# Kernel tuning notes

Hardware: AMD Instinct MI355X
Metric: run time of the kernel (lower is better)

Reference implementation:

```python
import jax, jax.numpy as jnp
import numpy as np

HEADS, KD, AR, RES, DIM = 8, 32, 4, 28, 384
D = AR * KD          # 128
DH = HEADS * D       # 1024
NH_KD = HEADS * KD   # 256


def setup_inputs() -> dict:
    key = jax.random.key(0)
    kit = iter(jax.random.split(key, 40))

    def rn(shape, scale=0.05):
        return jax.random.normal(next(kit), shape, jnp.float32) * scale

    B = 8
    inp = {}
    inp['x'] = jax.random.normal(next(kit), (B, DIM, RES, RES), jnp.float32)

    def conv_bn(name, o, i):
        # 1x1 conv weight [O, I] (kernel squeezed), conv bias, folded BN scale/shift
        inp['W' + name] = rn((o, i))
        inp['b' + name] = rn((o,))
        inp[name + '_s'] = 1.0 + rn((o,))
        inp[name + '_b'] = rn((o,))

    conv_bn('q', NH_KD, DIM)
    conv_bn('k', NH_KD, DIM)
    conv_bn('v', DH, DIM)
    # depthwise 3x3 v_local conv (OIHW, groups=DH -> I=1) + BN
    inp['Wvl'] = rn((DH, 1, 3, 3))
    inp['bvl'] = rn((DH,))
    inp['vl_s'] = 1.0 + rn((DH,))
    inp['vl_b'] = rn((DH,))
    # talking-head 1x1 convs over the heads axis: weight [out_head, in_head]
    inp['Wth1'] = rn((HEADS, HEADS))
    inp['bth1'] = rn((HEADS,))
    inp['Wth2'] = rn((HEADS, HEADS))
    inp['bth2'] = rn((HEADS,))
    conv_bn('p', DIM, DH)
    # relative position biases: one slot per unique (|dr|,|dc|) offset = RES*RES slots
    inp['attention_biases'] = rn((HEADS, RES * RES))
    r = np.arange(RES)
    rr, cc = np.meshgrid(r, r, indexing='ij')
    rows, cols = rr.reshape(-1), cc.reshape(-1)
    dr = np.abs(rows[:, None] - rows[None, :])
    dc = np.abs(cols[:, None] - cols[None, :])
    inp['bias_idxs'] = jnp.asarray(dr * RES + dc, jnp.int32)  # [N, N]
    return inp


def _cbn(t, W, b, s, sh):
    # 1x1 conv + eval-mode BatchNorm folded to per-channel affine
    y = jnp.einsum('bchw,oc->bohw', t, W) + b[None, :, None, None]
    return y * s[None, :, None, None] + sh[None, :, None, None]


def _forward(x, Wq, bq, q_s, q_b, Wk, bk, k_s, k_b, Wv, bv, v_s, v_b,
             Wvl, bvl, vl_s, vl_b, Wth1, bth1, Wth2, bth2,
             Wp, bp, p_s, p_b, attention_biases, bias_idxs):
    B, C, H, W = x.shape
    N = H * W
    scale = KD ** -0.5

    q = _cbn(x, Wq, bq, q_s, q_b).reshape(B, HEADS, KD, N).transpose(0, 1, 3, 2)  # [B,h,N,kd]
    k = _cbn(x, Wk, bk, k_s, k_b).reshape(B, HEADS, KD, N)                        # [B,h,kd,N]
    v4 = _cbn(x, Wv, bv, v_s, v_b)                                                # [B,dh,H,W]

    vl = jax.lax.conv_general_dilated(
        v4, Wvl, window_strides=(1, 1), padding='SAME',
        feature_group_count=DH, dimension_numbers=('NCHW', 'OIHW', 'NCHW'))
    vl = (vl + bvl[None, :, None, None]) * vl_s[None, :, None, None] + vl_b[None, :, None, None]

    v = v4.reshape(B, HEADS, D, N).transpose(0, 1, 3, 2)  # [B,h,N,d]

    ab = attention_biases[:, bias_idxs]                   # [h,N,N]
    attn = jnp.einsum('bhnk,bhkm->bhnm', q, k) * scale + ab[None]
    attn = jnp.einsum('bhnm,gh->bgnm', attn, Wth1) + bth1[None, :, None, None]
    attn = jax.nn.softmax(attn, axis=-1)
    attn = jnp.einsum('bhnm,gh->bgnm', attn, Wth2) + bth2[None, :, None, None]

    o = jnp.einsum('bhnm,bhmd->bhnd', attn, v)            # [B,h,N,d]
    o = o.transpose(0, 1, 3, 2).reshape(B, DH, H, W)
    o = o + vl
    return _cbn(o, Wp, bp, p_s, p_b)                      # [B,dim,H,W]


def reference(x, Wq, bq, q_s, q_b, Wk, bk, k_s, k_b, Wv, bv, v_s, v_b,
              Wvl, bvl, vl_s, vl_b, Wth1, bth1, Wth2, bth2,
              Wp, bp, p_s, p_b, attention_biases, bias_idxs):
    return _forward(x, Wq, bq, q_s, q_b, Wk, bk, k_s, k_b, Wv, bv, v_s, v_b,
                    Wvl, bvl, vl_s, vl_b, Wth1, bth1, Wth2, bth2,
                    Wp, bp, p_s, p_b, attention_biases, bias_idxs)
```

## Files before the change

kernel.cpp:

```cpp
#include <hip/hip_runtime.h>
#include <hip/hip_bf16.h>

typedef __hip_bfloat16 bf16;
typedef __attribute__((ext_vector_type(8))) short short8v;
typedef __attribute__((ext_vector_type(4))) short short4v;
typedef __attribute__((ext_vector_type(4))) float f32x4;
typedef __attribute__((ext_vector_type(2))) float f32x2;

__device__ __forceinline__ float b2f(bf16 v){ return __bfloat162float(v); }
__device__ __forceinline__ bf16  f2b(float v){ return __float2bfloat16(v); }
__device__ __forceinline__ float su2f(short s){
    unsigned short us = (unsigned short)s;
    return __bfloat162float(*reinterpret_cast<bf16*>(&us));
}
__device__ __forceinline__ float ldf(const void* t, size_t i, int isb){
    return isb ? b2f(((const bf16*)t)[i]) : ((const float*)t)[i];
}

constexpr int Bn = 8, CIN = 384, RESn = 28, Nn = 784, DHn = 1024;
constexpr int AST = 800;

__device__ __forceinline__ void gload16(const void* g, void* l)
{
    __builtin_amdgcn_global_load_lds(
        (const __attribute__((address_space(1))) void*)g,
        (__attribute__((address_space(3))) void*)l, 16, 0, 0);
}

__global__ void k_detect(const unsigned* __restrict__ xw, int* __restrict__ flag)
{
    if (blockIdx.x == 0 && threadIdx.x == 0) {
        int cnt = 0;
        for (int i = 0; i < 256; ++i) {
            unsigned lo = xw[i] & 0xFFFFu;
            int e = (int)((lo >> 7) & 0xFF);
            if (e >= 112 && e <= 132) ++cnt;
        }
        *flag = (cnt >= 128) ? 1 : 0;
    }
}

struct PtrArgs { const void* p[26]; };
__global__ __launch_bounds__(256) void k_prep(PtrArgs a, bf16* __restrict__ Wqkv,
                                              float* __restrict__ al, float* __restrict__ be,
                                              float* __restrict__ mb, bf16* __restrict__ Wvlt,
                                              const int* __restrict__ flag)
{
    const int isb = *flag;
    const int tid = threadIdx.x;
    const int role = blockIdx.y;
    if (role == 0) {
        int stride = gridDim.x * 256;
        for (int e = blockIdx.x * 256 + tid; e < 1536 * 384; e += stride) {
            int co = e / 384, k = e % 384;
            const void* src; int lc;
            if (co < 256)      { src = a.p[1]; lc = co; }
            else if (co < 512) { src = a.p[5]; lc = co - 256; }
            else               { src = a.p[9]; lc = co - 512; }
            Wqkv[e] = f2b(ldf(src, (size_t)lc * 384 + k, isb));
        }
    } else if (role == 1) {
        int co = blockIdx.x * 256 + tid;
        if (co < 1536) {
            const void *b_, *s_, *h_; int lc;
            if (co < 256)      { b_ = a.p[2];  s_ = a.p[3];  h_ = a.p[4];  lc = co; }
            else if (co < 512) { b_ = a.p[6];  s_ = a.p[7];  h_ = a.p[8];  lc = co - 256; }
            else               { b_ = a.p[10]; s_ = a.p[11]; h_ = a.p[12]; lc = co - 512; }
            float aa = ldf(s_, lc, isb);
            al[co] = aa;
            be[co] = ldf(b_, lc, isb) * aa + ldf(h_, lc, isb);
        }
    } else if (role == 2) {
        int i = blockIdx.x * 256 + tid;
        if (i < 8 * Nn) {
            int g = i / Nn, p = i % Nn;
            float acc = ldf(a.p[18], g, isb);
            #pragma unroll
            for (int h = 0; h < 8; ++h)
                acc += ldf(a.p[17], g * 8 + h, isb) * ldf(a.p[25], (size_t)h * Nn + p, isb);
            mb[i] = acc;
        }
    } else {
        int e = blockIdx.x * 256 + tid;
        if (e < 1024 * 9) {
            int c = e / 9, tap = e % 9;
            Wvlt[tap * 1024 + c] = f2b(ldf(a.p[13], e, isb));
        }
    }
}

struct ConvArgs { const void* src[10]; unsigned long long dstoff[10]; int n[10]; };
__global__ void k_convb_all(ConvArgs a, char* __restrict__ ws, const int* __restrict__ flag)
{
    int i = blockIdx.y;
    int n = a.n[i];
    const void* s = a.src[i];
    bf16* d = (bf16*)(ws + a.dstoff[i]);
    int isb = *flag;
    int stride = gridDim.x * blockDim.x;
    for (int t = blockIdx.x * blockDim.x + threadIdx.x; t < n; t += stride)
        d[t] = isb ? ((const bf16*)s)[t] : f2b(((const float*)s)[t]);
}

__global__ __launch_bounds__(256) void k_abfull(
    const float* __restrict__ mb, const int* __restrict__ idxs,
    bf16* __restrict__ abfull)
{
    __shared__ float mbs[8][Nn];
    const int tid = threadIdx.x;
    for (int i = tid; i < 8 * Nn; i += 256) ((float*)mbs)[i] = mb[i];
    __syncthreads();
    const int nstart = blockIdx.x * 2;
    for (int n = nstart; n < nstart + 2; ++n) {
        for (int m = tid; m < Nn; m += 256) {
            int id = idxs[(size_t)n * Nn + m];
            #pragma unroll
            for (int g = 0; g < 8; ++g)
                abfull[((size_t)g * Nn + n) * AST + m] = f2b(mbs[g][id]);
        }
    }
}

__global__ __launch_bounds__(256) void k_xt(const void* __restrict__ xr, bf16* __restrict__ xt,
                                            const int* __restrict__ flag)
{
    const int isb = *flag;
    __shared__ bf16 t[32][33];
    int b = blockIdx.z, n0 = blockIdx.x * 32, c0 = blockIdx.y * 32;
    int tid = threadIdx.x;
    for (int i = tid; i < 1024; i += 256) {
        int r = i >> 5, c = i & 31;
        int n = n0 + c;
        t[r][c] = (n < Nn) ? f2b(ldf(xr, ((size_t)b * CIN + c0 + r) * Nn + n, isb)) : f2b(0.f);
    }
    __syncthreads();
    for (int i = tid; i < 1024; i += 256) {
        int r = i >> 5, c = i & 31;
        int n = n0 + r;
        if (n < Nn) xt[((size_t)b * Nn + n) * CIN + c0 + c] = t[c][r];
    }
}

__global__ __launch_bounds__(256) void k_vt(const bf16* __restrict__ vbuf, bf16* __restrict__ vt)
{
    __shared__ bf16 t[32][33];
    int b = blockIdx.z, n0 = blockIdx.x * 32, c0 = blockIdx.y * 32;
    int tid = threadIdx.x;
    for (int i = tid; i < 1024; i += 256) {
        int r = i >> 5, c = i & 31;
        int n = n0 + r;
        t[r][c] = (n < Nn) ? vbuf[((size_t)b * Nn + n) * DHn + c0 + c] : f2b(0.f);
    }
    __syncthreads();
    for (int i = tid; i < 1024; i += 256) {
        int r = i >> 5, c = i & 31;
        int n = n0 + c;
        vt[((size_t)b * DHn + c0 + r) * AST + n] = t[c][r];
    }
}

template<int MI>
__device__ __forceinline__ void gemm_core(
    const bf16* __restrict__ A, int lda, int rowsA, int arow0,
    const bf16* __restrict__ B, int ldb, int rowsB, int brow0,
    int K, short* ldsA, short* ldsB, f32x4 (&acc)[MI][4])
{
    const int tid  = threadIdx.x;
    const int lane = tid & 63;
    const int wm   = tid >> 7, wn = (tid >> 6) & 1;
    const int rsub = ((tid >> 6) << 4) | (tid & 15);
    const int q    = (tid >> 4) & 3;
    const int wbase = tid & 192;
    const short8v* A8 = (const short8v*)ldsA;
    const short8v* B8 = (const short8v*)ldsB;

    for (int k0 = 0; k0 < K; k0 += 32) {
        __syncthreads();
        #pragma unroll
        for (int c = 0; c < MI / 2; ++c) {
            int row = arow0 + c * 64 + rsub; row = row < rowsA ? row : rowsA - 1;
            gload16((const short*)A + (size_t)row * lda + k0 + q * 8,
                    ldsA + (size_t)(c * 256 + wbase) * 8);
        }
        #pragma unroll
        for (int c = 0; c < 2; ++c) {
            int row = brow0 + c * 64 + rsub; row = row < rowsB ? row : rowsB - 1;
            gload16((const short*)B + (size_t)row * ldb + k0 + q * 8,
                    ldsB + (size_t)(c * 256 + wbase) * 8);
        }
        __syncthreads();
        short8v a[MI], bb[4];
        #pragma unroll
        for (int i = 0; i < MI; ++i) a[i] = A8[(wm * MI + i) * 64 + lane];
        #pragma unroll
        for (int j = 0; j < 4; ++j) bb[j] = B8[(wn * 4 + j) * 64 + lane];
        #pragma unroll
        for (int i = 0; i < MI; ++i)
            #pragma unroll
            for (int j = 0; j < 4; ++j)
                acc[i][j] = __builtin_amdgcn_mfma_f32_16x16x32_bf16(a[i], bb[j], acc[i][j], 0, 0, 0);
    }
}

#define EPI_COORDS(MI)                                      \
    const int tid  = threadIdx.x;                           \
    const int lane = tid & 63;                              \
    const int wm   = tid >> 7, wn = (tid >> 6) & 1;         \
    const int rq   = lane >> 4, cl = lane & 15; (void)rq;

__global__ __launch_bounds__(256) void k_proj_m(
    const bf16* __restrict__ xt, const bf16* __restrict__ Wqkv,
    const float* __restrict__ al, const float* __restrict__ be,
    bf16* __restrict__ qbuf, bf16* __restrict__ kbuf, bf16* __restrict__ vbuf)
{
    __shared__ short ldsA[4096], ldsB[4096];
    const int n0 = blockIdx.x * 128, co0 = blockIdx.y * 128;
    const int b = blockIdx.z;
    f32x4 acc[4][4] = {};
    gemm_core<4>(xt + (size_t)b * Nn * CIN, CIN, Nn, n0,
                 Wqkv, CIN, 1536, co0, CIN, ldsA, ldsB, acc);
    EPI_COORDS(4)
    #pragma unroll
    for (int i = 0; i < 4; ++i)
        #pragma unroll
        for (int j = 0; j < 4; ++j) {
            int co = co0 + (wn * 4 + j) * 16 + cl;
            float a_ = al[co], bb_ = be[co];
            int nb = n0 + (wm * 4 + i) * 16 + rq * 4;
            #pragma unroll
            for (int r = 0; r < 4; ++r) {
                int n = nb + r;
                if (n >= Nn) continue;
                float y = a_ * acc[i][j][r] + bb_;
                if (co < 256)      qbuf[((size_t)b * Nn + n) * 256 + co]       = f2b(y);
                else if (co < 512) kbuf[((size_t)b * Nn + n) * 256 + (co-256)] = f2b(y);
                else               vbuf[((size_t)b * Nn + n) * DHn + (co-512)] = f2b(y);
            }
        }
}

__global__ __launch_bounds__(256) void k_logits_raw(
    const bf16* __restrict__ qbuf, const bf16* __restrict__ kbuf,
    bf16* __restrict__ attn, int bi0)
{
    __shared__ short ldsA[4096], ldsB[4096];
    const int n0 = blockIdx.x * 128, m0 = blockIdx.y * 128;
    const int z = blockIdx.z, h = z & 7, bloc = z >> 3, b = bi0 + bloc;
    f32x4 acc[4][4] = {};
    gemm_core<4>(qbuf + (size_t)b * Nn * 256 + h * 32, 256, Nn, n0,
                 kbuf + (size_t)b * Nn * 256 + h * 32, 256, Nn, m0,
                 32, ldsA, ldsB, acc);
    bf16* arow = attn + (size_t)(bloc * 8 + h) * Nn * AST;
    EPI_COORDS(4)
    #pragma unroll
    for (int i = 0; i < 4; ++i)
        #pragma unroll
        for (int j = 0; j < 4; ++j) {
            int m = m0 + (wn * 4 + j) * 16 + cl;
            if (m >= Nn) continue;
            int nb = n0 + (wm * 4 + i) * 16 + rq * 4;
            #pragma unroll
            for (int r = 0; r < 4; ++r) {
                int n = nb + r;
                if (n < Nn) arow[(size_t)n * AST + m] = f2b(acc[i][j][r]);
            }
        }
}

__global__ __launch_bounds__(256) void k_softmax_mix(
    bf16* __restrict__ attn_all, const bf16* __restrict__ abfull,
    const bf16* __restrict__ W1, const bf16* __restrict__ W2, const bf16* __restrict__ b2v)
{
    const int n = blockIdx.x, bloc = blockIdx.y;
    const int tid = threadIdx.x;
    bf16* base = attn_all + (size_t)bloc * 8 * Nn * AST;
    __shared__ float w1s[64], w2s[64], b2sh[8], lis[8], wred[4][8];
    if (tid < 64) { w1s[tid] = b2f(W1[tid]) * 0.17677669529663687f; w2s[tid] = b2f(W2[tid]); }
    if (tid < 8)  b2sh[tid] = b2f(b2v[tid]);
    __syncthreads();

    const bool live = tid < 196;
    const int m0 = (live ? tid : 195) * 4;

    f32x2 raw2[8][2];
    #pragma unroll
    for (int h = 0; h < 8; ++h) {
        short4v v = *(const short4v*)(base + ((size_t)h * Nn + n) * AST + m0);
        raw2[h][0] = f32x2{su2f(v[0]), su2f(v[1])};
        raw2[h][1] = f32x2{su2f(v[2]), su2f(v[3])};
    }

    float out[8][4];
    #pragma unroll
    for (int g = 0; g < 8; ++g) {
        short4v bv = *(const short4v*)(abfull + ((size_t)g * Nn + n) * AST + m0);
        f32x2 a0 = {su2f(bv[0]), su2f(bv[1])};
        f32x2 a1 = {su2f(bv[2]), su2f(bv[3])};
        #pragma unroll
        for (int h = 0; h < 8; ++h) {
            float w = w1s[g * 8 + h];
            f32x2 wv = {w, w};
            a0 += raw2[h][0] * wv;
            a1 += raw2[h][1] * wv;
        }
        out[g][0] = __expf(fminf(a0[0], 60.f));
        out[g][1] = __expf(fminf(a0[1], 60.f));
        out[g][2] = __expf(fminf(a1[0], 60.f));
        out[g][3] = __expf(fminf(a1[1], 60.f));
        float s = live ? (out[g][0] + out[g][1]) + (out[g][2] + out[g][3]) : 0.f;
        #pragma unroll
        for (int sh = 32; sh > 0; sh >>= 1) s += __shfl_xor(s, sh, 64);
        if ((tid & 63) == 0) wred[tid >> 6][g] = s;
    }
    __syncthreads();
    if (tid < 8)
        lis[tid] = 1.f / (wred[0][tid] + wred[1][tid] + wred[2][tid] + wred[3][tid]);
    __syncthreads();

    f32x2 p2[8][2];
    #pragma unroll
    for (int h = 0; h < 8; ++h) {
        float lh = lis[h];
        p2[h][0] = f32x2{out[h][0] * lh, out[h][1] * lh};
        p2[h][1] = f32x2{out[h][2] * lh, out[h][3] * lh};
    }
    if (live) {
        #pragma unroll
        for (int g = 0; g < 8; ++g) {
            f32x2 acc0 = {b2sh[g], b2sh[g]};
            f32x2 acc1 = acc0;
            #pragma unroll
            for (int h = 0; h < 8; ++h) {
                float w = w2s[g * 8 + h];
                f32x2 wv = {w, w};
                acc0 += p2[h][0] * wv;
                acc1 += p2[h][1] * wv;
            }
            short4v sv;
            bf16 b0 = f2b(acc0[0]); sv[0] = *reinterpret_cast<short*>(&b0);
            bf16 b1 = f2b(acc0[1]); sv[1] = *reinterpret_cast<short*>(&b1);
            bf16 b2 = f2b(acc1[0]); sv[2] = *reinterpret_cast<short*>(&b2);
            bf16 b3 = f2b(acc1[1]); sv[3] = *reinterpret_cast<short*>(&b3);
            *(short4v*)(base + ((size_t)g * Nn + n) * AST + m0) = sv;
        }
    }
}

__global__ __launch_bounds__(256) void k_pv_m(
    const bf16* __restrict__ attn, const bf16* __restrict__ vt,
    bf16* __restrict__ obuf, int bi0)
{
    __shared__ short ldsA[2048], ldsB[4096];
    const int n0 = blockIdx.x * 64;
    const int z = blockIdx.z, g = z & 7, bloc = z >> 3, b = bi0 + bloc;
    f32x4 acc[2][4] = {};
    gemm_core<2>(attn + (size_t)(bloc * 8 + g) * Nn * AST, AST, Nn, n0,
                 vt + ((size_t)b * DHn + g * 128) * AST, AST, 128, 0,
                 AST, ldsA, ldsB, acc);
    bf16* ob = obuf + (size_t)b * Nn * DHn + g * 128;
    EPI_COORDS(2)
    #pragma unroll
    for (int i = 0; i < 2; ++i)
        #pragma unroll
        for (int j = 0; j < 4; ++j) {
            int d = (wn * 4 + j) * 16 + cl;
            int nb = n0 + (wm * 2 + i) * 16 + rq * 4;
            #pragma unroll
            for (int r = 0; r < 4; ++r) {
                int n = nb + r;
                if (n < Nn) ob[(size_t)n * DHn + d] = f2b(acc[i][j][r]);
            }
        }
}

__global__ __launch_bounds__(256) void k_dwconv_add(
    const bf16* __restrict__ vbuf, const bf16* __restrict__ Wvlt,
    const bf16* __restrict__ bvl, const bf16* __restrict__ vls, const bf16* __restrict__ vlb,
    bf16* __restrict__ obuf)
{
    const int t = threadIdx.x;
    const int n = blockIdx.y * 2 + (t >> 7);
    const int bi = blockIdx.z;
    const int c0 = (t & 127) * 8;
    const int h = n / RESn, w = n % RESn;
    float acc[8] = {};
    #pragma unroll
    for (int dh = -1; dh <= 1; ++dh)
        #pragma unroll
        for (int dw = -1; dw <= 1; ++dw) {
            int hh = h + dh, ww = w + dw;
            if (hh < 0 || hh >= RESn || ww < 0 || ww >= RESn) continue;
            int widx = (dh + 1) * 3 + (dw + 1);
            short8v wv = *(const short8v*)&Wvlt[widx * 1024 + c0];
            short8v v  = *(const short8v*)&vbuf[((size_t)bi * Nn + hh * RESn + ww) * DHn + c0];
            #pragma unroll
            for (int u = 0; u < 8; ++u)
                acc[u] += su2f(wv[u]) * su2f(v[u]);
        }
    short8v bv = *(const short8v*)&bvl[c0];
    short8v sv = *(const short8v*)&vls[c0];
    short8v hv = *(const short8v*)&vlb[c0];
    size_t off = ((size_t)bi * Nn + n) * DHn + c0;
    short8v ov = *(short8v*)&obuf[off];
    short8v res;
    #pragma unroll
    for (int u = 0; u < 8; ++u) {
        float vl = su2f(sv[u]) * (acc[u] + su2f(bv[u])) + su2f(hv[u]);
        bf16 bo = f2b(su2f(ov[u]) + vl);
        res[u] = *reinterpret_cast<short*>(&bo);
    }
    *(short8v*)&obuf[off] = res;
}

__global__ __launch_bounds__(256) void k_outproj_m(
    const bf16* __restrict__ Wp, const bf16* __restrict__ obuf,
    const bf16* __restrict__ bp, const bf16* __restrict__ ps, const bf16* __restrict__ pb,
    void* __restrict__ outv, const int* __restrict__ flag)
{
    __shared__ short ldsA[2048], ldsB[4096];
    const int n0 = blockIdx.x * 128, oc0 = blockIdx.y * 64;
    const int b = blockIdx.z;
    f32x4 acc[2][4] = {};
    gemm_core<2>(Wp, DHn, 384, oc0,
                 obuf + (size_t)b * Nn * DHn, DHn, Nn, n0,
                 DHn, ldsA, ldsB, acc);
    const int isb = *flag;
    EPI_COORDS(2)
    #pragma unroll
    for (int i = 0; i < 2; ++i)
        #pragma unroll
        for (int j = 0; j < 4; ++j) {
            int n = n0 + (wn * 4 + j) * 16 + cl;
            if (n >= Nn) continue;
            int ocb = oc0 + (wm * 2 + i) * 16 + rq * 4;
            #pragma unroll
            for (int r = 0; r < 4; ++r) {
                int oc = ocb + r;
                float a_ = b2f(ps[oc]);
                float be_ = b2f(bp[oc]) * a_ + b2f(pb[oc]);
                float y = a_ * acc[i][j][r] + be_;
                size_t idx = ((size_t)b * CIN + oc) * Nn + n;
                if (isb) ((bf16*)outv)[idx] = f2b(y);
                else     ((float*)outv)[idx] = y;
            }
        }
}

extern "C" void kernel_launch(void* const* d_in, const int* in_sizes, int n_in,
                              void* d_out, int out_size, void* d_ws, size_t ws_size,
                              hipStream_t stream)
{
    char* ws = (char*)d_ws;
    auto align256 = [](size_t v) { return (v + 255) & ~(size_t)255; };

    size_t off = 0;
    size_t off_flag = off;            off = align256(off + 4);
    size_t p_off[26];
    for (int i = 0; i < 26; ++i) { p_off[i] = off; off = align256(off + (size_t)in_sizes[i] * 2); }
    size_t off_mb   = off; off = align256(off + (size_t)8 * Nn * 4);
    size_t off_ab   = off; off = align256(off + (size_t)8 * Nn * AST * 2);
    size_t off_q    = off; off = align256(off + (size_t)Bn * Nn * 256 * 2);
    size_t off_k    = off; off = align256(off + (size_t)Bn * Nn * 256 * 2);
    size_t off_v    = off; off = align256(off + (size_t)Bn * Nn * DHn * 2);
    size_t off_vt   = off; off = align256(off + (size_t)Bn * DHn * AST * 2);
    size_t off_o    = off; off = align256(off + (size_t)Bn * Nn * DHn * 2);
    size_t off_xt   = off; off = align256(off + (size_t)Bn * Nn * CIN * 2);
    size_t off_wqkv = off; off = align256(off + (size_t)1536 * CIN * 2);
    size_t off_al   = off; off = align256(off + (size_t)1536 * 4);
    size_t off_be   = off; off = align256(off + (size_t)1536 * 4);
    size_t off_wvlt = off; off = align256(off + (size_t)9 * 1024 * 2);
    size_t base = off;

    const size_t attn_per_b = (size_t)8 * Nn * AST * 2;
    int GB = 0;
    const int cand[4] = {8, 4, 2, 1};
    for (int ci = 0; ci < 4; ++ci) {
        if (base + (size_t)cand[ci] * attn_per_b + 512 <= ws_size) { GB = cand[ci]; break; }
    }
    if (!GB) return;

    size_t off_attn = base;

    int*  flag = (int*)(ws + off_flag);
    bf16* Pb[26];
    for (int i = 0; i < 26; ++i) Pb[i] = (bf16*)(ws + p_off[i]);
    float* mb    = (float*)(ws + off_mb);
    bf16* abfull = (bf16*)(ws + off_ab);
    bf16* qbuf  = (bf16*)(ws + off_q);
    bf16* kbuf  = (bf16*)(ws + off_k);
    bf16* vbuf  = (bf16*)(ws + off_v);
    bf16* vt    = (bf16*)(ws + off_vt);
    bf16* obuf  = (bf16*)(ws + off_o);
    bf16* xt    = (bf16*)(ws + off_xt);
    bf16* wqkv  = (bf16*)(ws + off_wqkv);
    float* alf  = (float*)(ws + off_al);
    float* bef  = (float*)(ws + off_be);
    bf16* wvlt  = (bf16*)(ws + off_wvlt);
    bf16* attn  = (bf16*)(ws + off_attn);
    const int* idxs = (const int*)d_in[26];

    k_detect<<<1, 64, 0, stream>>>((const unsigned*)d_in[0], flag);

    PtrArgs pa;
    for (int i = 0; i < 26; ++i) pa.p[i] = d_in[i];
    k_prep<<<dim3(288, 4), 256, 0, stream>>>(pa, wqkv, alf, bef, mb, wvlt, flag);

    const int cidx[10] = {14, 15, 16, 17, 19, 20, 21, 22, 23, 24};
    ConvArgs ca;
    for (int i = 0; i < 10; ++i) {
        ca.src[i] = d_in[cidx[i]];
        ca.dstoff[i] = p_off[cidx[i]];
        ca.n[i] = in_sizes[cidx[i]];
    }
    k_convb_all<<<dim3(64, 10), 256, 0, stream>>>(ca, ws, flag);

    bf16 *bvl = Pb[14], *vls = Pb[15], *vlb = Pb[16],
         *W1 = Pb[17], *W2 = Pb[19], *b2v = Pb[20],
         *Wp = Pb[21], *bp = Pb[22], *ps = Pb[23], *pb = Pb[24];

    k_xt<<<dim3(25, 12, 8), 256, 0, stream>>>(d_in[0], xt, flag);
    k_abfull<<<dim3(392), 256, 0, stream>>>(mb, idxs, abfull);

    k_proj_m<<<dim3(7, 12, 8), 256, 0, stream>>>(xt, wqkv, alf, bef, qbuf, kbuf, vbuf);
    k_vt<<<dim3(25, 32, 8), 256, 0, stream>>>(vbuf, vt);

    for (int bi0 = 0; bi0 < Bn; bi0 += GB) {
        k_logits_raw<<<dim3(7, 7, GB * 8), 256, 0, stream>>>(qbuf, kbuf, attn, bi0);
        k_softmax_mix<<<dim3(Nn, GB), 256, 0, stream>>>(attn, abfull, W1, W2, b2v);
        k_pv_m<<<dim3(13, 1, GB * 8), 256, 0, stream>>>(attn, vt, obuf, bi0);
    }

    k_dwconv_add<<<dim3(1, Nn / 2, 8), 256, 0, stream>>>(vbuf, wvlt, bvl, vls, vlb, obuf);
    k_outproj_m<<<dim3(7, 6, 8), 256, 0, stream>>>(Wp, obuf, bp, ps, pb, d_out, flag);
}
```

Measured before the change: 238.5 us.

## Fuse logits with talking-head mix and exp; fuse normalize and second mix into PV

The old three-kernel attention pipeline was logits, a separate softmax/mix pass and PV. It becomes two kernels. The first computes QK^T for all heads of a 16-row tile, applies the first talking-head mix with bias and exp, writes unnormalized exponentials, and writes partial row sums. The second normalizes using the split sums, applies the second head mix while staging P into LDS, and runs the PV MFMA. This removes one full read and write pass over the large attention buffer and one launch. The cost is smaller, more redundant tiles (E is reread per group pair) and a changed LDS staging layout.

Result: slower. 408.7 us (+71.4%).

```diff
diff --git a/kernel.cpp b/kernel.cpp
--- a/kernel.cpp
+++ b/kernel.cpp
@@ -5,13 +5,16 @@
 typedef __attribute__((ext_vector_type(8))) short short8v;
 typedef __attribute__((ext_vector_type(4))) short short4v;
 typedef __attribute__((ext_vector_type(4))) float f32x4;
-typedef __attribute__((ext_vector_type(2))) float f32x2;
 
 __device__ __forceinline__ float b2f(bf16 v){ return __bfloat162float(v); }
 __device__ __forceinline__ bf16  f2b(float v){ return __float2bfloat16(v); }
 __device__ __forceinline__ float su2f(short s){
     unsigned short us = (unsigned short)s;
     return __bfloat162float(*reinterpret_cast<bf16*>(&us));
+}
+__device__ __forceinline__ short f2s(float v){
+    bf16 b = __float2bfloat16(v);
+    return *reinterpret_cast<short*>(&b);
 }
 __device__ __forceinline__ float ldf(const void* t, size_t i, int isb){
     return isb ? b2f(((const bf16*)t)[i]) : ((const float*)t)[i];
@@ -159,6 +162,16 @@
     }
 }
 
+__device__ __forceinline__ void stage64x32(const bf16* __restrict__ src,
+    int row0, int row_lim, int k0, int k_lim, int ld, short* lds, int tid)
+{
+    int rsub = ((tid >> 6) << 4) | (tid & 15);
+    int q    = (tid >> 4) & 3;
+    int row = row0 + rsub; row = row < row_lim ? row : row_lim - 1;
+    gload16((const short*)src + (size_t)row * ld + k0 + q * 8,
+            lds + (size_t)(((rsub >> 4) * 4 + q) * 16 + (rsub & 15)) * 8);
+}
+
 template<int MI>
 __device__ __forceinline__ void gemm_core(
     const bf16* __restrict__ A, int lda, int rowsA, int arow0,
@@ -168,26 +181,17 @@
     const int tid  = threadIdx.x;
     const int lane = tid & 63;
     const int wm   = tid >> 7, wn = (tid >> 6) & 1;
-    const int rsub = ((tid >> 6) << 4) | (tid & 15);
-    const int q    = (tid >> 4) & 3;
-    const int wbase = tid & 192;
     const short8v* A8 = (const short8v*)ldsA;
     const short8v* B8 = (const short8v*)ldsB;
 
     for (int k0 = 0; k0 < K; k0 += 32) {
         __syncthreads();
         #pragma unroll
-        for (int c = 0; c < MI / 2; ++c) {
-            int row = arow0 + c * 64 + rsub; row = row < rowsA ? row : rowsA - 1;
-            gload16((const short*)A + (size_t)row * lda + k0 + q * 8,
-                    ldsA + (size_t)(c * 256 + wbase) * 8);
-        }
-        #pragma unroll
-        for (int c = 0; c < 2; ++c) {
-            int row = brow0 + c * 64 + rsub; row = row < rowsB ? row : rowsB - 1;
-            gload16((const short*)B + (size_t)row * ldb + k0 + q * 8,
-                    ldsB + (size_t)(c * 256 + wbase) * 8);
-        }
+        for (int c = 0; c < MI / 2; ++c)
+            stage64x32(A, arow0 + c * 64, rowsA, k0, K, lda, ldsA + c * 2048, tid);
+        #pragma unroll
+        for (int c = 0; c < 2; ++c)
+            stage64x32(B, brow0 + c * 64, rowsB, k0, K, ldb, ldsB + c * 2048, tid);
         __syncthreads();
         short8v a[MI], bb[4];
         #pragma unroll
@@ -239,138 +243,197 @@
         }
 }
 
-__global__ __launch_bounds__(256) void k_logits_raw(
+__global__ __launch_bounds__(256) void k_attA(
     const bf16* __restrict__ qbuf, const bf16* __restrict__ kbuf,
-    bf16* __restrict__ attn, int bi0)
-{
-    __shared__ short ldsA[4096], ldsB[4096];
-    const int n0 = blockIdx.x * 128, m0 = blockIdx.y * 128;
-    const int z = blockIdx.z, h = z & 7, bloc = z >> 3, b = bi0 + bloc;
-    f32x4 acc[4][4] = {};
-    gemm_core<4>(qbuf + (size_t)b * Nn * 256 + h * 32, 256, Nn, n0,
-                 kbuf + (size_t)b * Nn * 256 + h * 32, 256, Nn, m0,
-                 32, ldsA, ldsB, acc);
-    bf16* arow = attn + (size_t)(bloc * 8 + h) * Nn * AST;
-    EPI_COORDS(4)
-    #pragma unroll
-    for (int i = 0; i < 4; ++i)
-        #pragma unroll
-        for (int j = 0; j < 4; ++j) {
-            int m = m0 + (wn * 4 + j) * 16 + cl;
-            if (m >= Nn) continue;
-            int nb = n0 + (wm * 4 + i) * 16 + rq * 4;
+    const bf16* __restrict__ abfull, const bf16* __restrict__ W1,
+    bf16* __restrict__ E, float* __restrict__ sums, int bi0)
+{
+    __shared__ short ldsQ[4096];
+    __shared__ short ldsK[16384];
+    __shared__ float sred[4][8][16];
+    __shared__ float w1s[64];
+    const int tid = threadIdx.x;
+    const int nt = blockIdx.x >> 1, ms = blockIdx.x & 1;
+    const int bloc = blockIdx.y, b = bi0 + bloc;
+    const int n0 = nt * 16;
+    const int lane = tid & 63, wv = tid >> 6;
+    const int qrow = lane >> 4, cl = lane & 15;
+
+    if (tid < 64) w1s[tid] = b2f(W1[tid]) * 0.17677669529663687f;
+
+    {
+        const short8v* q8 = (const short8v*)(qbuf + (size_t)b * Nn * 256);
+        short8v* Q8w = (short8v*)ldsQ;
+        #pragma unroll
+        for (int s = tid; s < 512; s += 256) {
+            int r = s >> 5, j = s & 31;
+            Q8w[(j >> 2) * 64 + (j & 3) * 16 + r] = q8[(size_t)(n0 + r) * 32 + j];
+        }
+    }
+
+    float sreg[8][4];
+    #pragma unroll
+    for (int g = 0; g < 8; ++g)
+        #pragma unroll
+        for (int r = 0; r < 4; ++r) sreg[g][r] = 0.f;
+
+    const bf16* Bk = kbuf + (size_t)b * Nn * 256;
+    const short8v* Q8 = (const short8v*)ldsQ;
+    const short8v* K8 = (const short8v*)ldsK;
+    const int nmt = 6 + ms;
+
+    for (int mt = 0; mt < nmt; ++mt) {
+        int m0 = ms * 384 + mt * 64;
+        __syncthreads();
+        #pragma unroll
+        for (int h = 0; h < 8; ++h)
+            stage64x32(Bk, m0, Nn, h * 32, 256, 256, ldsK + h * 2048, tid);
+        __syncthreads();
+        f32x4 acc[8];
+        #pragma unroll
+        for (int h = 0; h < 8; ++h) {
+            short8v a = Q8[h * 64 + lane];
+            short8v bb = K8[h * 256 + wv * 64 + lane];
+            f32x4 z = {0.f, 0.f, 0.f, 0.f};
+            acc[h] = __builtin_amdgcn_mfma_f32_16x16x32_bf16(a, bb, z, 0, 0, 0);
+        }
+        const int m = m0 + wv * 16 + cl;
+        #pragma unroll
+        for (int g = 0; g < 8; ++g) {
             #pragma unroll
             for (int r = 0; r < 4; ++r) {
-                int n = nb + r;
-                if (n < Nn) arow[(size_t)n * AST + m] = f2b(acc[i][j][r]);
+                int n = n0 + qrow * 4 + r;
+                float a = (m < AST) ?
+                    su2f(*(const short*)&abfull[((size_t)g * Nn + n) * AST + m]) : 0.f;
+                #pragma unroll
+                for (int h = 0; h < 8; ++h) a += w1s[g * 8 + h] * acc[h][r];
+                float e = (m < Nn) ? __expf(fminf(a, 60.f)) : 0.f;
+                sreg[g][r] += e;
+                if (m < AST)
+                    E[((size_t)(bloc * 8 + g) * Nn + n) * AST + m] = f2b(e);
             }
         }
-}
-
-__global__ __launch_bounds__(256) void k_softmax_mix(
-    bf16* __restrict__ attn_all, const bf16* __restrict__ abfull,
-    const bf16* __restrict__ W1, const bf16* __restrict__ W2, const bf16* __restrict__ b2v)
-{
-    const int n = blockIdx.x, bloc = blockIdx.y;
+    }
+
+    #pragma unroll
+    for (int g = 0; g < 8; ++g)
+        #pragma unroll
+        for (int r = 0; r < 4; ++r) {
+            float v = sreg[g][r];
+            v += __shfl_xor(v, 1, 64);
+            v += __shfl_xor(v, 2, 64);
+            v += __shfl_xor(v, 4, 64);
+            v += __shfl_xor(v, 8, 64);
+            if (cl == 0) sred[wv][g][qrow * 4 + r] = v;
+        }
+    __syncthreads();
+    if (tid < 128) {
+        int g = tid >> 4, nl = tid & 15;
+        float s = sred[0][g][nl] + sred[1][g][nl] + sred[2][g][nl] + sred[3][g][nl];
+        sums[(size_t)ms * 64 * Nn + (size_t)(bloc * 8 + g) * Nn + n0 + nl] = s;
+    }
+}
+
+__global__ __launch_bounds__(256) void k_attB(
+    const bf16* __restrict__ E, const float* __restrict__ sums,
+    const bf16* __restrict__ vt, const bf16* __restrict__ W2,
+    const bf16* __restrict__ b2v, bf16* __restrict__ obuf, int bi0)
+{
+    __shared__ short ldsP[2][2048];
+    __shared__ short ldsV[2][8192];
+    __shared__ float w2sh[2][8];
+    __shared__ float b2sh[2];
     const int tid = threadIdx.x;
-    bf16* base = attn_all + (size_t)bloc * 8 * Nn * AST;
-    __shared__ float w1s[64], w2s[64], b2sh[8], lis[8], wred[4][8];
-    if (tid < 64) { w1s[tid] = b2f(W1[tid]) * 0.17677669529663687f; w2s[tid] = b2f(W2[tid]); }
-    if (tid < 8)  b2sh[tid] = b2f(b2v[tid]);
+    const int nt = blockIdx.x, gp = blockIdx.y, bloc = blockIdx.z;
+    const int b = bi0 + bloc;
+    const int n0 = nt * 32;
+    const int g0 = gp * 2;
+    const int lane = tid & 63, wv = tid >> 6;
+
+    if (tid < 16) w2sh[tid >> 3][tid & 7] = b2f(W2[(g0 + (tid >> 3)) * 8 + (tid & 7)]);
+    if (tid < 2)  b2sh[tid] = b2f(b2v[g0 + tid]);
+
+    const int nrow = tid >> 3;
+    const int msg  = (tid & 7) * 8;
+    const int nclamp = (n0 + nrow < Nn) ? (n0 + nrow) : (Nn - 1);
+    float dinv[8];
+    #pragma unroll
+    for (int h = 0; h < 8; ++h) {
+        size_t idx = (size_t)(bloc * 8 + h) * Nn + nclamp;
+        dinv[h] = 1.f / (sums[idx] + sums[(size_t)64 * Nn + idx]);
+    }
     __syncthreads();
 
-    const bool live = tid < 196;
-    const int m0 = (live ? tid : 195) * 4;
-
-    f32x2 raw2[8][2];
-    #pragma unroll
-    for (int h = 0; h < 8; ++h) {
-        short4v v = *(const short4v*)(base + ((size_t)h * Nn + n) * AST + m0);
-        raw2[h][0] = f32x2{su2f(v[0]), su2f(v[1])};
-        raw2[h][1] = f32x2{su2f(v[2]), su2f(v[3])};
-    }
-
-    float out[8][4];
-    #pragma unroll
-    for (int g = 0; g < 8; ++g) {
-        short4v bv = *(const short4v*)(abfull + ((size_t)g * Nn + n) * AST + m0);
-        f32x2 a0 = {su2f(bv[0]), su2f(bv[1])};
-        f32x2 a1 = {su2f(bv[2]), su2f(bv[3])};
-        #pragma unroll
-        for (int h = 0; h < 8; ++h) {
-            float w = w1s[g * 8 + h];
-            f32x2 wv = {w, w};
-            a0 += raw2[h][0] * wv;
-            a1 += raw2[h][1] * wv;
-        }
-        out[g][0] = __expf(fminf(a0[0], 60.f));
-        out[g][1] = __expf(fminf(a0[1], 60.f));
-        out[g][2] = __expf(fminf(a1[0], 60.f));
-        out[g][3] = __expf(fminf(a1[1], 60.f));
-        float s = live ? (out[g][0] + out[g][1]) + (out[g][2] + out[g][3]) : 0.f;
-        #pragma unroll
-        for (int sh = 32; sh > 0; sh >>= 1) s += __shfl_xor(s, sh, 64);
-        if ((tid & 63) == 0) wred[tid >> 6][g] = s;
-    }
-    __syncthreads();
-    if (tid < 8)
-        lis[tid] = 1.f / (wred[0][tid] + wred[1][tid] + wred[2][tid] + wred[3][tid]);
-    __syncthreads();
-
-    f32x2 p2[8][2];
-    #pragma unroll
-    for (int h = 0; h < 8; ++h) {
-        float lh = lis[h];
-        p2[h][0] = f32x2{out[h][0] * lh, out[h][1] * lh};
-        p2[h][1] = f32x2{out[h][2] * lh, out[h][3] * lh};
-    }
-    if (live) {
-        #pragma unroll
-        for (int g = 0; g < 8; ++g) {
-            f32x2 acc0 = {b2sh[g], b2sh[g]};
-            f32x2 acc1 = acc0;
-            #pragma unroll
-            for (int h = 0; h < 8; ++h) {
-                float w = w2s[g * 8 + h];
-                f32x2 wv = {w, w};
-                acc0 += p2[h][0] * wv;
-                acc1 += p2[h][1] * wv;
+    f32x4 acc[2][2][2] = {};
+
+    for (int mt = 0; mt < 13; ++mt) {
+        const int m0 = mt * 64;
+        const int nks = (mt < 12) ? 2 : 1;
+        __syncthreads();
+        #pragma unroll
+        for (int gs = 0; gs < 2; ++gs) {
+            const bf16* vs = vt + ((size_t)b * DHn + (g0 + gs) * 128) * AST;
+            for (int ks = 0; ks < nks; ++ks) {
+                stage64x32(vs, 0,  128, m0 + ks * 32, AST, AST, ldsV[gs] + ks * 4096, tid);
+                stage64x32(vs, 64, 128, m0 + ks * 32, AST, AST, ldsV[gs] + ks * 4096 + 2048, tid);
             }
-            short4v sv;
-            bf16 b0 = f2b(acc0[0]); sv[0] = *reinterpret_cast<short*>(&b0);
-            bf16 b1 = f2b(acc0[1]); sv[1] = *reinterpret_cast<short*>(&b1);
-            bf16 b2 = f2b(acc1[0]); sv[2] = *reinterpret_cast<short*>(&b2);
-            bf16 b3 = f2b(acc1[1]); sv[3] = *reinterpret_cast<short*>(&b3);
-            *(short4v*)(base + ((size_t)g * Nn + n) * AST + m0) = sv;
-        }
-    }
-}
-
-__global__ __launch_bounds__(256) void k_pv_m(
-    const bf16* __restrict__ attn, const bf16* __restrict__ vt,
-    bf16* __restrict__ obuf, int bi0)
-{
-    __shared__ short ldsA[2048], ldsB[4096];
-    const int n0 = blockIdx.x * 64;
-    const int z = blockIdx.z, g = z & 7, bloc = z >> 3, b = bi0 + bloc;
-    f32x4 acc[2][4] = {};
-    gemm_core<2>(attn + (size_t)(bloc * 8 + g) * Nn * AST, AST, Nn, n0,
-                 vt + ((size_t)b * DHn + g * 128) * AST, AST, 128, 0,
-                 AST, ldsA, ldsB, acc);
-    bf16* ob = obuf + (size_t)b * Nn * DHn + g * 128;
-    EPI_COORDS(2)
-    #pragma unroll
-    for (int i = 0; i < 2; ++i)
-        #pragma unroll
-        for (int j = 0; j < 4; ++j) {
-            int d = (wn * 4 + j) * 16 + cl;
-            int nb = n0 + (wm * 2 + i) * 16 + rq * 4;
-            #pragma unroll
-            for (int r = 0; r < 4; ++r) {
-                int n = nb + r;
-                if (n < Nn) ob[(size_t)n * DHn + d] = f2b(acc[i][j][r]);
+        }
+        if (msg < nks * 32) {
+            float p0[8], p1[8];
+            #pragma unroll
+            for (int e = 0; e < 8; ++e) { p0[e] = b2sh[0]; p1[e] = b2sh[1]; }
+            #pragma unroll
+            for (int g = 0; g < 8; ++g) {
+                short8v ev = *(const short8v*)&E[
+                    ((size_t)(bloc * 8 + g) * Nn + nclamp) * AST + m0 + msg];
+                float w0 = w2sh[0][g], w1 = w2sh[1][g], dv = dinv[g];
+                #pragma unroll
+                for (int e = 0; e < 8; ++e) {
+                    float pe = su2f(ev[e]) * dv;
+                    p0[e] += w0 * pe;
+                    p1[e] += w1 * pe;
+                }
             }
-        }
+            short8v s0, s1;
+            #pragma unroll
+            for (int e = 0; e < 8; ++e) { s0[e] = f2s(p0[e]); s1[e] = f2s(p1[e]); }
+            int ks = msg >> 5, q = (msg >> 3) & 3, sub = nrow >> 4, r = nrow & 15;
+            int slot = (ks * 2 + sub) * 64 + q * 16 + r;
+            ((short8v*)ldsP[0])[slot] = s0;
+            ((short8v*)ldsP[1])[slot] = s1;
+        }
+        __syncthreads();
+        #pragma unroll
+        for (int gs = 0; gs < 2; ++gs)
+            for (int ks = 0; ks < nks; ++ks)
+                #pragma unroll
+                for (int sub = 0; sub < 2; ++sub) {
+                    short8v a = ((const short8v*)ldsP[gs])[(ks * 2 + sub) * 64 + lane];
+                    #pragma unroll
+                    for (int jj = 0; jj < 2; ++jj) {
+                        short8v bb = ((const short8v*)ldsV[gs])[ks * 512 + (wv * 2 + jj) * 64 + lane];
+                        acc[gs][sub][jj] =
+                            __builtin_amdgcn_mfma_f32_16x16x32_bf16(a, bb, acc[gs][sub][jj], 0, 0, 0);
+                    }
+                }
+    }
+
+    const int qrow = lane >> 4, cl = lane & 15;
+    #pragma unroll
+    for (int gs = 0; gs < 2; ++gs)
+        #pragma unroll
+        for (int sub = 0; sub < 2; ++sub)
+            #pragma unroll
+            for (int jj = 0; jj < 2; ++jj) {
+                int d = (g0 + gs) * 128 + (wv * 2 + jj) * 16 + cl;
+                int nb = n0 + sub * 16 + qrow * 4;
+                #pragma unroll
+                for (int r = 0; r < 4; ++r) {
+                    int n = nb + r;
+                    if (n < Nn)
+                        obuf[((size_t)b * Nn + n) * DHn + d] = f2b(acc[gs][sub][jj][r]);
+                }
+            }
 }
 
 __global__ __launch_bounds__(256) void k_dwconv_add(
@@ -406,8 +469,7 @@
     #pragma unroll
     for (int u = 0; u < 8; ++u) {
         float vl = su2f(sv[u]) * (acc[u] + su2f(bv[u])) + su2f(hv[u]);
-        bf16 bo = f2b(su2f(ov[u]) + vl);
-        res[u] = *reinterpret_cast<short*>(&bo);
+        res[u] = f2s(su2f(ov[u]) + vl);
     }
     *(short8v*)&obuf[off] = res;
 }
@@ -469,6 +531,7 @@
     size_t off_al   = off; off = align256(off + (size_t)1536 * 4);
     size_t off_be   = off; off = align256(off + (size_t)1536 * 4);
     size_t off_wvlt = off; off = align256(off + (size_t)9 * 1024 * 2);
+    size_t off_sums = off; off = align256(off + (size_t)2 * 64 * Nn * 4);
     size_t base = off;
 
     const size_t attn_per_b = (size_t)8 * Nn * AST * 2;
@@ -496,6 +559,7 @@
     float* alf  = (float*)(ws + off_al);
     float* bef  = (float*)(ws + off_be);
     bf16* wvlt  = (bf16*)(ws + off_wvlt);
+    float* sums = (float*)(ws + off_sums);
     bf16* attn  = (bf16*)(ws + off_attn);
     const int* idxs = (const int*)d_in[26];
 
@@ -525,9 +589,8 @@
     k_vt<<<dim3(25, 32, 8), 256, 0, stream>>>(vbuf, vt);
 
     for (int bi0 = 0; bi0 < Bn; bi0 += GB) {
-        k_logits_raw<<<dim3(7, 7, GB * 8), 256, 0, stream>>>(qbuf, kbuf, attn, bi0);
-        k_softmax_mix<<<dim3(Nn, GB), 256, 0, stream>>>(attn, abfull, W1, W2, b2v);
-        k_pv_m<<<dim3(13, 1, GB * 8), 256, 0, stream>>>(attn, vt, obuf, bi0);
+        k_attA<<<dim3(98, GB), 256, 0, stream>>>(qbuf, kbuf, abfull, W1, attn, sums, bi0);
+        k_attB<<<dim3(25, 4, GB), 256, 0, stream>>>(attn, sums, vt, W2, b2v, obuf, bi0);
     }
 
     k_dwconv_add<<<dim3(1, Nn / 2, 8), 256, 0, stream>>>(vbuf, wvlt, bvl, vls, vlb, obuf);
```

## Store mixed attention probabilities as 8-bit floats and fold talking-head bias via V column sums

Applied to the files above, without the earlier changes.

The softmax/mix kernel now writes the talking-head-mixed probabilities as e5m2-style 8-bit floats (the top byte of an fp16) into a separate buffer, without adding the second talking-head bias. The PV GEMM reads these bytes, widens them to bf16 in registers, stages them to LDS with plain stores, and adds bias times a precomputed per-channel column sum of V in the epilogue. The aim is to halve the bytes of the largest intermediate written by softmax and read by PV. In exchange the probabilities keep only two mantissa bits, which risks accuracy, and PV loses the asynchronous global-to-LDS load for its A operand. The extra buffer may also force smaller batch groups when workspace is tight.

After: 242.8 us. Within noise of the previous version (+1.8%).

```diff
diff --git a/kernel.cpp b/kernel.cpp
--- a/kernel.cpp
+++ b/kernel.cpp
@@ -1,5 +1,6 @@
 #include <hip/hip_runtime.h>
 #include <hip/hip_bf16.h>
+#include <hip/hip_fp16.h>
 
 typedef __hip_bfloat16 bf16;
 typedef __attribute__((ext_vector_type(8))) short short8v;
@@ -13,8 +14,20 @@
     unsigned short us = (unsigned short)s;
     return __bfloat162float(*reinterpret_cast<bf16*>(&us));
 }
+__device__ __forceinline__ short f2s(float v){
+    bf16 b = __float2bfloat16(v);
+    return *reinterpret_cast<short*>(&b);
+}
 __device__ __forceinline__ float ldf(const void* t, size_t i, int isb){
     return isb ? b2f(((const bf16*)t)[i]) : ((const float*)t)[i];
+}
+__device__ __forceinline__ unsigned f2bf8(float f){
+    unsigned short h = __half_as_ushort(__float2half(f));
+    unsigned lsb = (h >> 8) & 1u, rb = (h >> 7) & 1u, st = (h & 0x7Fu) ? 1u : 0u;
+    return ((unsigned)(h >> 8) + (rb & (st | lsb))) & 0xFFu;
+}
+__device__ __forceinline__ float bf82f(unsigned b){
+    return __half2float(__ushort_as_half((unsigned short)(b << 8)));
 }
 
 constexpr int Bn = 8, CIN = 384, RESn = 28, Nn = 784, DHn = 1024;
@@ -159,6 +172,32 @@
     }
 }
 
+__global__ __launch_bounds__(256) void k_vcolsum(
+    const bf16* __restrict__ vbuf, float* __restrict__ colsum)
+{
+    __shared__ float red[4][64];
+    const int b = blockIdx.y, c0 = blockIdx.x * 64;
+    const int t = threadIdx.x, cl = t & 63, part = t >> 6;
+    float s = 0.f;
+    const int nst = part * 196;
+    for (int n = nst; n < nst + 196; ++n)
+        s += b2f(vbuf[((size_t)b * Nn + n) * DHn + c0 + cl]);
+    red[part][cl] = s;
+    __syncthreads();
+    if (t < 64)
+        colsum[(size_t)b * DHn + c0 + t] = red[0][t] + red[1][t] + red[2][t] + red[3][t];
+}
+
+__device__ __forceinline__ void stage64x32(const bf16* __restrict__ src,
+    int row0, int row_lim, int k0, int k_lim, int ld, short* lds, int tid)
+{
+    int rsub = ((tid >> 6) << 4) | (tid & 15);
+    int q    = (tid >> 4) & 3;
+    int row = row0 + rsub; row = row < row_lim ? row : row_lim - 1;
+    gload16((const short*)src + (size_t)row * ld + k0 + q * 8,
+            lds + (size_t)(((rsub >> 4) * 4 + q) * 16 + (rsub & 15)) * 8);
+}
+
 template<int MI>
 __device__ __forceinline__ void gemm_core(
     const bf16* __restrict__ A, int lda, int rowsA, int arow0,
@@ -168,26 +207,17 @@
     const int tid  = threadIdx.x;
     const int lane = tid & 63;
     const int wm   = tid >> 7, wn = (tid >> 6) & 1;
-    const int rsub = ((tid >> 6) << 4) | (tid & 15);
-    const int q    = (tid >> 4) & 3;
-    const int wbase = tid & 192;
     const short8v* A8 = (const short8v*)ldsA;
     const short8v* B8 = (const short8v*)ldsB;
 
     for (int k0 = 0; k0 < K; k0 += 32) {
         __syncthreads();
         #pragma unroll
-        for (int c = 0; c < MI / 2; ++c) {
-            int row = arow0 + c * 64 + rsub; row = row < rowsA ? row : rowsA - 1;
-            gload16((const short*)A + (size_t)row * lda + k0 + q * 8,
-                    ldsA + (size_t)(c * 256 + wbase) * 8);
-        }
-        #pragma unroll
-        for (int c = 0; c < 2; ++c) {
-            int row = brow0 + c * 64 + rsub; row = row < rowsB ? row : rowsB - 1;
-            gload16((const short*)B + (size_t)row * ldb + k0 + q * 8,
-                    ldsB + (size_t)(c * 256 + wbase) * 8);
-        }
+        for (int c = 0; c < MI / 2; ++c)
+            stage64x32(A, arow0 + c * 64, rowsA, k0, K, lda, ldsA + c * 2048, tid);
+        #pragma unroll
+        for (int c = 0; c < 2; ++c)
+            stage64x32(B, brow0 + c * 64, rowsB, k0, K, ldb, ldsB + c * 2048, tid);
         __syncthreads();
         short8v a[MI], bb[4];
         #pragma unroll
@@ -268,15 +298,16 @@
 }
 
 __global__ __launch_bounds__(256) void k_softmax_mix(
-    bf16* __restrict__ attn_all, const bf16* __restrict__ abfull,
-    const bf16* __restrict__ W1, const bf16* __restrict__ W2, const bf16* __restrict__ b2v)
+    const bf16* __restrict__ attn_all, unsigned char* __restrict__ p2_all,
+    const bf16* __restrict__ abfull,
+    const bf16* __restrict__ W1, const bf16* __restrict__ W2)
 {
     const int n = blockIdx.x, bloc = blockIdx.y;
     const int tid = threadIdx.x;
-    bf16* base = attn_all + (size_t)bloc * 8 * Nn * AST;
-    __shared__ float w1s[64], w2s[64], b2sh[8], lis[8], wred[4][8];
+    const bf16* base = attn_all + (size_t)bloc * 8 * Nn * AST;
+    unsigned char* p2b = p2_all + (size_t)bloc * 8 * Nn * AST;
+    __shared__ float w1s[64], w2s[64], lis[8], wred[4][8];
     if (tid < 64) { w1s[tid] = b2f(W1[tid]) * 0.17677669529663687f; w2s[tid] = b2f(W2[tid]); }
-    if (tid < 8)  b2sh[tid] = b2f(b2v[tid]);
     __syncthreads();
 
     const bool live = tid < 196;
@@ -327,8 +358,8 @@
     if (live) {
         #pragma unroll
         for (int g = 0; g < 8; ++g) {
-            f32x2 acc0 = {b2sh[g], b2sh[g]};
-            f32x2 acc1 = acc0;
+            f32x2 acc0 = {0.f, 0.f};
+            f32x2 acc1 = {0.f, 0.f};
             #pragma unroll
             for (int h = 0; h < 8; ++h) {
                 float w = w2s[g * 8 + h];
@@ -336,39 +367,76 @@
                 acc0 += p2[h][0] * wv;
                 acc1 += p2[h][1] * wv;
             }
-            short4v sv;
-            bf16 b0 = f2b(acc0[0]); sv[0] = *reinterpret_cast<short*>(&b0);
-            bf16 b1 = f2b(acc0[1]); sv[1] = *reinterpret_cast<short*>(&b1);
-            bf16 b2 = f2b(acc1[0]); sv[2] = *reinterpret_cast<short*>(&b2);
-            bf16 b3 = f2b(acc1[1]); sv[3] = *reinterpret_cast<short*>(&b3);
-            *(short4v*)(base + ((size_t)g * Nn + n) * AST + m0) = sv;
+            unsigned u = f2bf8(acc0[0]) | (f2bf8(acc0[1]) << 8)
+                       | (f2bf8(acc1[0]) << 16) | (f2bf8(acc1[1]) << 24);
+            *(unsigned*)(p2b + ((size_t)g * Nn + n) * AST + m0) = u;
         }
     }
 }
 
 __global__ __launch_bounds__(256) void k_pv_m(
-    const bf16* __restrict__ attn, const bf16* __restrict__ vt,
+    const unsigned char* __restrict__ p2, const bf16* __restrict__ vt,
+    const bf16* __restrict__ b2v, const float* __restrict__ colsum,
     bf16* __restrict__ obuf, int bi0)
 {
     __shared__ short ldsA[2048], ldsB[4096];
+    const int tid = threadIdx.x;
     const int n0 = blockIdx.x * 64;
     const int z = blockIdx.z, g = z & 7, bloc = z >> 3, b = bi0 + bloc;
+    const unsigned char* Ap = p2 + (size_t)(bloc * 8 + g) * Nn * AST;
+    const bf16* Bv = vt + ((size_t)b * DHn + g * 128) * AST;
+    const int lane = tid & 63;
+    const int wm = tid >> 7, wn = (tid >> 6) & 1;
+    const int rsub = ((tid >> 6) << 4) | (tid & 15);
+    const int q = (tid >> 4) & 3;
+    const short8v* A8 = (const short8v*)ldsA;
+    const short8v* B8 = (const short8v*)ldsB;
     f32x4 acc[2][4] = {};
-    gemm_core<2>(attn + (size_t)(bloc * 8 + g) * Nn * AST, AST, Nn, n0,
-                 vt + ((size_t)b * DHn + g * 128) * AST, AST, 128, 0,
-                 AST, ldsA, ldsB, acc);
+
+    for (int k0 = 0; k0 < AST; k0 += 32) {
+        __syncthreads();
+        {
+            int row = n0 + rsub; row = row < Nn ? row : Nn - 1;
+            const unsigned char* src = Ap + (size_t)row * AST + k0 + q * 8;
+            unsigned lo = *(const unsigned*)src;
+            unsigned hi = *(const unsigned*)(src + 4);
+            short8v o;
+            #pragma unroll
+            for (int j = 0; j < 4; ++j) {
+                o[j]     = f2s(bf82f((lo >> (8 * j)) & 0xFFu));
+                o[4 + j] = f2s(bf82f((hi >> (8 * j)) & 0xFFu));
+            }
+            ((short8v*)ldsA)[((rsub >> 4) * 4 + q) * 16 + (rsub & 15)] = o;
+        }
+        stage64x32(Bv, 0,  128, k0, AST, AST, ldsB, tid);
+        stage64x32(Bv, 64, 128, k0, AST, AST, ldsB + 2048, tid);
+        __syncthreads();
+        short8v a[2], bb[4];
+        #pragma unroll
+        for (int i = 0; i < 2; ++i) a[i] = A8[(wm * 2 + i) * 64 + lane];
+        #pragma unroll
+        for (int j = 0; j < 4; ++j) bb[j] = B8[(wn * 4 + j) * 64 + lane];
+        #pragma unroll
+        for (int i = 0; i < 2; ++i)
+            #pragma unroll
+            for (int j = 0; j < 4; ++j)
+                acc[i][j] = __builtin_amdgcn_mfma_f32_16x16x32_bf16(a[i], bb[j], acc[i][j], 0, 0, 0);
+    }
+
     bf16* ob = obuf + (size_t)b * Nn * DHn + g * 128;
-    EPI_COORDS(2)
+    const float b2g = b2f(b2v[g]);
+    const int rq = lane >> 4, cl = lane & 15;
     #pragma unroll
     for (int i = 0; i < 2; ++i)
         #pragma unroll
         for (int j = 0; j < 4; ++j) {
             int d = (wn * 4 + j) * 16 + cl;
+            float cs = b2g * colsum[(size_t)b * DHn + g * 128 + d];
             int nb = n0 + (wm * 2 + i) * 16 + rq * 4;
             #pragma unroll
             for (int r = 0; r < 4; ++r) {
                 int n = nb + r;
-                if (n < Nn) ob[(size_t)n * DHn + d] = f2b(acc[i][j][r]);
+                if (n < Nn) ob[(size_t)n * DHn + d] = f2b(acc[i][j][r] + cs);
             }
         }
 }
@@ -406,8 +474,7 @@
     #pragma unroll
     for (int u = 0; u < 8; ++u) {
         float vl = su2f(sv[u]) * (acc[u] + su2f(bv[u])) + su2f(hv[u]);
-        bf16 bo = f2b(su2f(ov[u]) + vl);
-        res[u] = *reinterpret_cast<short*>(&bo);
+        res[u] = f2s(su2f(ov[u]) + vl);
     }
     *(short8v*)&obuf[off] = res;
 }
@@ -469,17 +536,20 @@
     size_t off_al   = off; off = align256(off + (size_t)1536 * 4);
     size_t off_be   = off; off = align256(off + (size_t)1536 * 4);
     size_t off_wvlt = off; off = align256(off + (size_t)9 * 1024 * 2);
+    size_t off_cs   = off; off = align256(off + (size_t)Bn * DHn * 4);
     size_t base = off;
 
     const size_t attn_per_b = (size_t)8 * Nn * AST * 2;
+    const size_t p2_per_b   = (size_t)8 * Nn * AST;
     int GB = 0;
     const int cand[4] = {8, 4, 2, 1};
     for (int ci = 0; ci < 4; ++ci) {
-        if (base + (size_t)cand[ci] * attn_per_b + 512 <= ws_size) { GB = cand[ci]; break; }
+        if (base + (size_t)cand[ci] * (attn_per_b + p2_per_b) + 512 <= ws_size) { GB = cand[ci]; break; }
     }
     if (!GB) return;
 
     size_t off_attn = base;
+    size_t off_p2   = align256(off_attn + (size_t)GB * attn_per_b);
 
     int*  flag = (int*)(ws + off_flag);
     bf16* Pb[26];
@@ -496,7 +566,9 @@
     float* alf  = (float*)(ws + off_al);
     float* bef  = (float*)(ws + off_be);
     bf16* wvlt  = (bf16*)(ws + off_wvlt);
+    float* csum = (float*)(ws + off_cs);
     bf16* attn  = (bf16*)(ws + off_attn);
+    unsigned char* p2b = (unsigned char*)(ws + off_p2);
     const int* idxs = (const int*)d_in[26];
 
     k_detect<<<1, 64, 0, stream>>>((const unsigned*)d_in[0], flag);
@@ -523,11 +595,12 @@
 
     k_proj_m<<<dim3(7, 12, 8), 256, 0, stream>>>(xt, wqkv, alf, bef, qbuf, kbuf, vbuf);
     k_vt<<<dim3(25, 32, 8), 256, 0, stream>>>(vbuf, vt);
+    k_vcolsum<<<dim3(16, 8), 256, 0, stream>>>(vbuf, csum);
 
     for (int bi0 = 0; bi0 < Bn; bi0 += GB) {
         k_logits_raw<<<dim3(7, 7, GB * 8), 256, 0, stream>>>(qbuf, kbuf, attn, bi0);
-        k_softmax_mix<<<dim3(Nn, GB), 256, 0, stream>>>(attn, abfull, W1, W2, b2v);
-        k_pv_m<<<dim3(13, 1, GB * 8), 256, 0, stream>>>(attn, vt, obuf, bi0);
+        k_softmax_mix<<<dim3(Nn, GB), 256, 0, stream>>>(attn, p2b, abfull, W1, W2);
+        k_pv_m<<<dim3(13, 1, GB * 8), 256, 0, stream>>>(p2b, vt, b2v, csum, obuf, bi0);
     }
 
     k_dwconv_add<<<dim3(1, Nn / 2, 8), 256, 0, stream>>>(vbuf, wvlt, bvl, vls, vlb, obuf);
```
